# Performance work log

Measured on AMD Instinct MI355X. Metric: run time of the kernel, lower is better.

## Reference

```python
import jax, jax.numpy as jnp
import numpy as np
import math

B, L, D, H, FF = 32, 512, 512, 8, 2048
DH = D // H
EPS = 1e-5

def pe_table(L, D):
    pos = jnp.arange(L, dtype=jnp.float32)[:, None]
    div = jnp.exp(jnp.arange(0, D, 2, dtype=jnp.float32) * (-(math.log(10000.0) / D)))
    pe = jnp.zeros((L, D), dtype=jnp.float32)
    pe = pe.at[:, 0::2].set(jnp.sin(pos * div))
    pe = pe.at[:, 1::2].set(jnp.cos(pos * div))
    return pe

def setup_inputs() -> dict:
    key = jax.random.key(0)
    ks = jax.random.split(key, 16)
    s = 0.02
    inp = {
        "x": jax.random.normal(ks[0], (B, L, D), jnp.float32),
        "mask": jnp.ones((B, L), jnp.int32),
        "speaker_emb": jax.random.normal(ks[1], (B, L, D), jnp.float32),
        "Wg": jax.random.normal(ks[2], (D, D), jnp.float32) * s,
        "Wq": jax.random.normal(ks[3], (D, D), jnp.float32) * s,
        "bq": jnp.zeros((D,), jnp.float32),
        "Wk": jax.random.normal(ks[4], (D, D), jnp.float32) * s,
        "bk": jnp.zeros((D,), jnp.float32),
        "Wv": jax.random.normal(ks[5], (D, D), jnp.float32) * s,
        "bv": jnp.zeros((D,), jnp.float32),
        "Wo": jax.random.normal(ks[6], (D, D), jnp.float32) * s,
        "bo": jnp.zeros((D,), jnp.float32),
        "ln_g": jnp.ones((D,), jnp.float32),
        "ln_b": jnp.zeros((D,), jnp.float32),
        "W1": jax.random.normal(ks[7], (FF, D), jnp.float32) * s,
        "b1": jnp.zeros((FF,), jnp.float32),
        "W2": jax.random.normal(ks[8], (D, FF), jnp.float32) * s,
        "b2": jnp.zeros((D,), jnp.float32),
    }
    return inp

def layer_norm(x, g, b):
    mu = jnp.mean(x, axis=-1, keepdims=True)
    var = jnp.var(x, axis=-1, keepdims=True)
    return (x - mu) * jax.lax.rsqrt(var + EPS) * g + b

def reference(x, mask, speaker_emb, Wg, Wq, bq, Wk, bk, Wv, bv, Wo, bo, ln_g, ln_b, W1, b1, W2, b2):
    # DynamicGating: sigmoid(x W^T) * x
    x = jax.nn.sigmoid(x @ Wg.T) * x
    # speaker embedding + sinusoidal positional encoding (dropout is eval/no-op)
    x = x + speaker_emb + pe_table(L, D)[None, :, :]
    # Multi-head self-attention (eager, full score matrix)
    q = (x @ Wq.T + bq).reshape(B, L, H, DH).transpose(0, 2, 1, 3) / math.sqrt(DH)
    k = (x @ Wk.T + bk).reshape(B, L, H, DH).transpose(0, 2, 1, 3)
    v = (x @ Wv.T + bv).reshape(B, L, H, DH).transpose(0, 2, 1, 3)
    scores = jnp.einsum("bhqd,bhkd->bhqk", q, k)  # (B,H,L,L)
    key_mask = (mask == 0)[:, None, None, :]  # mask keys where mask==0
    scores = jnp.where(key_mask, jnp.float32(-1e10), scores)
    attn = jax.nn.softmax(scores, axis=-1)
    ctx = jnp.einsum("bhqk,bhkd->bhqd", attn, v)
    ctx = ctx.transpose(0, 2, 1, 3).reshape(B, L, D)
    attn_out = ctx @ Wo.T + bo
    h = attn_out + x  # residual (dropout no-op)
    # FeedForwardNet: note GELU applied after BOTH linears (faithful to source)
    mid = jax.nn.gelu(layer_norm(h, ln_g, ln_b) @ W1.T + b1, approximate=True)
    out = jax.nn.gelu(mid @ W2.T + b2, approximate=True)
    return out + h
```

## Files before the change

### kernel.cpp

```cpp
#include <hip/hip_runtime.h>
#include <math.h>

#define Bn 32
#define Ln 512
#define Dn 512
#define Hn 8
#define DHn 64
#define FFn 2048
#define Mn (Bn*Ln)
#define QKVS 1536

typedef __attribute__((ext_vector_type(4))) float f32x4;
typedef __attribute__((ext_vector_type(8))) short short8;

__device__ __forceinline__ float bf2f(ushort u){ return __uint_as_float(((unsigned)u) << 16); }
__device__ __forceinline__ ushort f2bf(float f){
  unsigned u = __float_as_uint(f);
  u += 0x7FFFu + ((u >> 16) & 1u);
  return (ushort)(u >> 16);
}
__device__ __forceinline__ float gelu_fast(float x){
  float y2 = 1.5957691216057308f * (x + 0.044715f*x*x*x);
  return x / (1.0f + __expf(-y2));
}

__device__ __forceinline__ void gload_lds16(const ushort* g, ushort* l){
  __builtin_amdgcn_global_load_lds(
      (__attribute__((address_space(1))) void*)(void*)g,
      (__attribute__((address_space(3))) void*)(void*)l, 16, 0, 0);
}

__device__ __forceinline__ void cvt4(const float* __restrict__ in, ushort* __restrict__ out, int u){
  float4 v = *(const float4*)(in + u*4);
  ushort4 o;
  o.x = f2bf(v.x); o.y = f2bf(v.y); o.z = f2bf(v.z); o.w = f2bf(v.w);
  *(ushort4*)(out + u*4) = o;
}

__global__ __launch_bounds__(256) void prep_kernel(
    const float* __restrict__ Wg, const float* __restrict__ Wq, const float* __restrict__ Wk,
    const float* __restrict__ Wv, const float* __restrict__ Wo, const float* __restrict__ W1,
    const float* __restrict__ W2,
    const float* __restrict__ bq, const float* __restrict__ bk, const float* __restrict__ bv,
    ushort* __restrict__ wgb, ushort* __restrict__ wqkvb, ushort* __restrict__ wob,
    ushort* __restrict__ w1b, ushort* __restrict__ w2b,
    float* __restrict__ pe, float* __restrict__ bqkv)
{
  int u = blockIdx.x*256 + threadIdx.x;
  const int WU = 65536, FU = 262144;
  if (u < WU){ cvt4(Wg, wgb, u); return; }            u -= WU;
  if (u < WU){ cvt4(Wq, wqkvb, u); return; }          u -= WU;
  if (u < WU){ cvt4(Wk, wqkvb + 262144, u); return; } u -= WU;
  if (u < WU){ cvt4(Wv, wqkvb + 524288, u); return; } u -= WU;
  if (u < WU){ cvt4(Wo, wob, u); return; }            u -= WU;
  if (u < FU){ cvt4(W1, w1b, u); return; }            u -= FU;
  if (u < FU){ cvt4(W2, w2b, u); return; }            u -= FU;
  if (u < WU){
    int e = u*4; int l = e >> 9; int d0 = e & 511;
    #pragma unroll
    for (int p=0;p<2;p++){
      int i = (d0 >> 1) + p;
      float dv = expf((float)(2*i) * (-9.210340371976184f/512.0f));
      float ang = (float)l * dv;
      pe[e + 2*p]     = sinf(ang);
      pe[e + 2*p + 1] = cosf(ang);
    }
    return;
  }
  u -= WU;
  if (u < 384){
    int e = u*4;
    #pragma unroll
    for (int j=0;j<4;j++){
      int i = e + j;
      bqkv[i] = (i < 512) ? bq[i] : (i < 1024) ? bk[i-512] : bv[i-1024];
    }
  }
}

__global__ void cvt_kernel(const float* __restrict__ in, ushort* __restrict__ out, int n){
  int i = (blockIdx.x*256 + threadIdx.x)*4;
  if (i >= n) return;
  cvt4(in, out, i >> 2);
}

template<int MODE>
__global__ __launch_bounds__(256) void gemm_kernel(
    const ushort* __restrict__ A, const ushort* __restrict__ W,
    const float* __restrict__ bias,
    const float* __restrict__ res,
    const float* __restrict__ spk, const float* __restrict__ pe,
    float* __restrict__ outf, ushort* __restrict__ outb, ushort* __restrict__ outb2,
    int K, int N, int gx)
{
  __shared__ ushort lA[2][128][64];
  __shared__ ushort lW[2][128][64];
  int t = threadIdx.x;
  int wave = t >> 6, lane = t & 63;
  int wr = wave >> 1, wc = wave & 1;
  int g = lane >> 4, r16 = lane & 15;

  int nwg = gx * (Mn/128);
  int wg = blockIdx.x;
  int tile = (wg & 7)*(nwg >> 3) + (wg >> 3);
  int trow = tile / gx;
  int tcol = tile - trow*gx;
  int rowBase = trow * 128;
  int colBase = tcol * 128;

  int srow8 = lane >> 3;
  int sucol = ((lane & 7) ^ srow8) * 8;
  const ushort* gA = A + (size_t)(rowBase + wave*8 + srow8)*K + sucol;
  const ushort* gW = W + (size_t)(colBase + wave*8 + srow8)*K + sucol;

  f32x4 acc[4][4];
  #pragma unroll
  for (int m=0;m<4;m++)
    #pragma unroll
    for (int n=0;n<4;n++) acc[m][n] = (f32x4)0.0f;

  {
    ushort* la = &lA[0][0][0] + wave*512;
    ushort* lw = &lW[0][0][0] + wave*512;
    #pragma unroll
    for (int c=0;c<4;c++){
      gload_lds16(gA + (size_t)c*32*K, la + c*2048);
      gload_lds16(gW + (size_t)c*32*K, lw + c*2048);
    }
  }

  int cb = 0;
  for (int k0 = 0; k0 < K; k0 += 64){
    if (k0 + 64 < K){
      ushort* la = &lA[cb^1][0][0] + wave*512;
      ushort* lw = &lW[cb^1][0][0] + wave*512;
      #pragma unroll
      for (int c=0;c<4;c++){
        gload_lds16(gA + (size_t)c*32*K + k0 + 64, la + c*2048);
        gload_lds16(gW + (size_t)c*32*K + k0 + 64, lw + c*2048);
      }
      asm volatile("s_waitcnt vmcnt(8)" ::: "memory");
    } else {
      asm volatile("s_waitcnt vmcnt(0)" ::: "memory");
    }
    __builtin_amdgcn_s_barrier();
    #pragma unroll
    for (int ks=0; ks<2; ks++){
      short8 af[4], bfr[4];
      #pragma unroll
      for (int m=0;m<4;m++){
        int row = wr*64 + m*16 + r16;
        af[m] = *(const short8*)&lA[cb][row][(((ks<<2)+g) ^ (r16 & 7))*8];
      }
      #pragma unroll
      for (int n=0;n<4;n++){
        int row = wc*64 + n*16 + r16;
        bfr[n] = *(const short8*)&lW[cb][row][(((ks<<2)+g) ^ (r16 & 7))*8];
      }
      #pragma unroll
      for (int m=0;m<4;m++)
        #pragma unroll
        for (int n=0;n<4;n++)
          acc[m][n] = __builtin_amdgcn_mfma_f32_16x16x32_bf16(af[m], bfr[n], acc[m][n], 0, 0, 0);
    }
    __builtin_amdgcn_s_barrier();
    cb ^= 1;
  }

  if constexpr (MODE == 1 || MODE == 3){
    bool vpart = false;
    if constexpr (MODE == 1) vpart = (colBase >= 1024);
    if (!vpart){
      ushort* ct = &lA[0][0][0];
      #pragma unroll
      for (int m=0;m<4;m++){
        #pragma unroll
        for (int n=0;n<4;n++){
          int col = wc*64 + n*16 + r16;
          int gc = colBase + col;
          float sc = 1.0f;
          if constexpr (MODE == 1) sc = (gc < 512) ? 0.125f : 1.0f;
          #pragma unroll
          for (int j=0;j<4;j++){
            int row = wr*64 + m*16 + g*4 + j;
            float c = acc[m][n][j] + bias[gc];
            ushort val;
            if constexpr (MODE == 3) val = f2bf(gelu_fast(c));
            else                     val = f2bf(c * sc);
            ct[row*128 + (col ^ ((row & 7) << 3))] = val;
          }
        }
      }
      __syncthreads();
      int r = t >> 1, ch = (t & 1)*64;
      ushort* dst = outb + (size_t)(rowBase + r)*N + colBase + ch;
      #pragma unroll
      for (int q=0;q<8;q++){
        int col = (ch + q*8) ^ ((r & 7) << 3);
        *(short8*)(dst + q*8) = *(const short8*)&ct[r*128 + col];
      }
    } else {
      #pragma unroll
      for (int m=0;m<4;m++){
        #pragma unroll
        for (int n=0;n<4;n++){
          int gc = colBase + wc*64 + n*16 + r16;
          int dhg = gc - 1024;
          int gr0 = rowBase + wr*64 + m*16 + g*4;
          int bb = gr0 >> 9, l0 = gr0 & 511;
          ushort4 o4;
          o4.x = f2bf(acc[m][n][0] + bias[gc]);
          o4.y = f2bf(acc[m][n][1] + bias[gc]);
          o4.z = f2bf(acc[m][n][2] + bias[gc]);
          o4.w = f2bf(acc[m][n][3] + bias[gc]);
          *(ushort4*)(outb2 + ((size_t)(bb*Hn + (dhg>>6))*DHn + (dhg & 63))*Ln + l0) = o4;
        }
      }
    }
  } else {
    #pragma unroll
    for (int m=0;m<4;m++){
      #pragma unroll
      for (int n=0;n<4;n++){
        int gc = colBase + wc*64 + n*16 + r16;
        #pragma unroll
        for (int j=0;j<4;j++){
          int gr = rowBase + wr*64 + m*16 + g*4 + j;
          size_t o = (size_t)gr * N + gc;
          float c = acc[m][n][j];
          if constexpr (MODE == 0){
            float s = 1.0f/(1.0f + __expf(-c));
            float rv = s * res[o] + spk[o] + pe[(gr & (Ln-1))*Dn + gc];
            outf[o] = rv; outb[o] = f2bf(rv);
          } else if constexpr (MODE == 2){
            outf[o] = c + bias[gc] + res[o];
          } else {
            outf[o] = gelu_fast(c + bias[gc]) + res[o];
          }
        }
      }
    }
  }
}

__global__ __launch_bounds__(256) void attn_mfma_kernel(
    const ushort* __restrict__ qb, const ushort* __restrict__ kb, const ushort* __restrict__ vtb,
    const int* __restrict__ mask, ushort* __restrict__ ctxb)
{
  __shared__ ushort lK[2][64][72];
  __shared__ ushort lVt[2][64][72];
  __shared__ ushort lP[4][32][72];

  int t = threadIdx.x;
  int w = t >> 6, lane = t & 63;
  int g = lane >> 4, r16 = lane & 15;
  int b = blockIdx.z, h = blockIdx.y;
  int qbase = blockIdx.x*128 + w*32;

  int key0 = t >> 3;
  int c8s = (t & 7) * 8;
  const ushort* kbase = kb + (size_t)(b*Ln)*QKVS + h*DHn + c8s;
  const ushort* vt = vtb + (size_t)((b*Hn + h)*DHn) * Ln;

  short8 af_q[2][2];
  #pragma unroll
  for (int m=0;m<2;m++)
    #pragma unroll
    for (int ks=0;ks<2;ks++)
      af_q[m][ks] = *(const short8*)(qb + (size_t)(b*Ln + qbase + m*16 + r16)*QKVS + h*DHn + ks*32 + g*8);

  f32x4 acc_ctx[2][4];
  #pragma unroll
  for (int m=0;m<2;m++)
    #pragma unroll
    for (int n=0;n<4;n++) acc_ctx[m][n] = (f32x4)0.0f;
  float mrun[2][4], lrun[2][4];
  #pragma unroll
  for (int m=0;m<2;m++)
    #pragma unroll
    for (int j=0;j<4;j++){ mrun[m][j] = -INFINITY; lrun[m][j] = 0.0f; }

  {
    short8 ka = *(const short8*)(kbase + (size_t)key0*QKVS);
    short8 kc = *(const short8*)(kbase + (size_t)(key0+32)*QKVS);
    short8 va = *(const short8*)(vt + (size_t)key0*Ln + c8s);
    short8 vc = *(const short8*)(vt + (size_t)(key0+32)*Ln + c8s);
    *(short8*)&lK[0][key0][c8s] = ka;
    *(short8*)&lK[0][key0+32][c8s] = kc;
    *(short8*)&lVt[0][key0][c8s] = va;
    *(short8*)&lVt[0][key0+32][c8s] = vc;
  }
  __syncthreads();
  int cb = 0;

  for (int kb0 = 0; kb0 < Ln; kb0 += 64){
    short8 kna, knb, vna, vnb;
    bool more = (kb0 + 64 < Ln);
    if (more){
      kna = *(const short8*)(kbase + (size_t)(kb0 + 64 + key0)*QKVS);
      knb = *(const short8*)(kbase + (size_t)(kb0 + 64 + key0 + 32)*QKVS);
      vna = *(const short8*)(vt + (size_t)key0*Ln + kb0 + 64 + c8s);
      vnb = *(const short8*)(vt + (size_t)(key0+32)*Ln + kb0 + 64 + c8s);
    }

    f32x4 acc_s[2][4];
    #pragma unroll
    for (int m=0;m<2;m++)
      #pragma unroll
      for (int n=0;n<4;n++) acc_s[m][n] = (f32x4)0.0f;
    __builtin_amdgcn_s_setprio(1);
    #pragma unroll
    for (int ks=0;ks<2;ks++){
      short8 bf_k[4];
      #pragma unroll
      for (int n=0;n<4;n++)
        bf_k[n] = *(const short8*)&lK[cb][n*16 + r16][ks*32 + g*8];
      #pragma unroll
      for (int m=0;m<2;m++)
        #pragma unroll
        for (int n=0;n<4;n++)
          acc_s[m][n] = __builtin_amdgcn_mfma_f32_16x16x32_bf16(af_q[m][ks], bf_k[n], acc_s[m][n], 0, 0, 0);
    }
    __builtin_amdgcn_s_setprio(0);

    #pragma unroll
    for (int n=0;n<4;n++){
      if (mask[b*Ln + kb0 + n*16 + r16] == 0){
        #pragma unroll
        for (int m=0;m<2;m++)
          #pragma unroll
          for (int j=0;j<4;j++) acc_s[m][n][j] = -1e10f;
      }
    }

    #pragma unroll
    for (int m=0;m<2;m++){
      #pragma unroll
      for (int j=0;j<4;j++){
        float tmax = fmaxf(fmaxf(acc_s[m][0][j], acc_s[m][1][j]),
                           fmaxf(acc_s[m][2][j], acc_s[m][3][j]));
        #pragma unroll
        for (int off=1; off<16; off<<=1) tmax = fmaxf(tmax, __shfl_xor(tmax, off));
        float newm = fmaxf(mrun[m][j], tmax);
        float alpha = __expf(mrun[m][j] - newm);
        float p0 = __expf(acc_s[m][0][j] - newm);
        float p1 = __expf(acc_s[m][1][j] - newm);
        float p2 = __expf(acc_s[m][2][j] - newm);
        float p3 = __expf(acc_s[m][3][j] - newm);
        float tsum = (p0+p1)+(p2+p3);
        #pragma unroll
        for (int off=1; off<16; off<<=1) tsum += __shfl_xor(tsum, off);
        lrun[m][j] = lrun[m][j]*alpha + tsum;
        mrun[m][j] = newm;
        #pragma unroll
        for (int n2=0;n2<4;n2++) acc_ctx[m][n2][j] *= alpha;
        int prow = m*16 + g*4 + j;
        lP[w][prow][0*16 + r16] = f2bf(p0);
        lP[w][prow][1*16 + r16] = f2bf(p1);
        lP[w][prow][2*16 + r16] = f2bf(p2);
        lP[w][prow][3*16 + r16] = f2bf(p3);
      }
    }

    __builtin_amdgcn_s_setprio(1);
    #pragma unroll
    for (int ks2=0;ks2<2;ks2++){
      short8 af_p[2], bf_v[4];
      #pragma unroll
      for (int m=0;m<2;m++)
        af_p[m] = *(const short8*)&lP[w][m*16 + r16][ks2*32 + g*8];
      #pragma unroll
      for (int n=0;n<4;n++)
        bf_v[n] = *(const short8*)&lVt[cb][n*16 + r16][ks2*32 + g*8];
      #pragma unroll
      for (int m=0;m<2;m++)
        #pragma unroll
        for (int n=0;n<4;n++)
          acc_ctx[m][n] = __builtin_amdgcn_mfma_f32_16x16x32_bf16(af_p[m], bf_v[n], acc_ctx[m][n], 0, 0, 0);
    }
    __builtin_amdgcn_s_setprio(0);

    if (more){
      *(short8*)&lK[cb^1][key0][c8s] = kna;
      *(short8*)&lK[cb^1][key0+32][c8s] = knb;
      *(short8*)&lVt[cb^1][key0][c8s] = vna;
      *(short8*)&lVt[cb^1][key0+32][c8s] = vnb;
    }
    __syncthreads();
    cb ^= 1;
  }

  #pragma unroll
  for (int m=0;m<2;m++){
    #pragma unroll
    for (int j=0;j<4;j++){
      float inv = 1.0f / lrun[m][j];
      int gr = qbase + m*16 + g*4 + j;
      #pragma unroll
      for (int n=0;n<4;n++){
        ctxb[(size_t)(b*Ln + gr)*Dn + h*DHn + n*16 + r16] = f2bf(acc_ctx[m][n][j] * inv);
      }
    }
  }
}

__global__ __launch_bounds__(256) void ln_kernel(
    const float* __restrict__ hbuf, const float* __restrict__ gamma, const float* __restrict__ beta,
    ushort* __restrict__ out)
{
  int row = blockIdx.x*4 + (threadIdx.x >> 6);
  int lane = threadIdx.x & 63;
  const float* p = hbuf + (size_t)row*Dn + lane*8;
  float4 a = *(const float4*)p;
  float4 c = *(const float4*)(p + 4);
  float v[8] = {a.x,a.y,a.z,a.w,c.x,c.y,c.z,c.w};
  float s = 0.f, ss = 0.f;
  #pragma unroll
  for (int j=0;j<8;j++){ s += v[j]; ss += v[j]*v[j]; }
  #pragma unroll
  for (int off=32; off>0; off>>=1){ s += __shfl_xor(s, off); ss += __shfl_xor(ss, off); }
  float mu = s * (1.0f/Dn);
  float var = ss * (1.0f/Dn) - mu*mu;
  float rstd = rsqrtf(var + 1e-5f);
  ushort o8[8];
  #pragma unroll
  for (int j=0;j<8;j++) o8[j] = f2bf((v[j]-mu)*rstd*gamma[lane*8+j] + beta[lane*8+j]);
  ushort* op = out + (size_t)row*Dn + lane*8;
  *(ushort4*)op       = make_ushort4(o8[0],o8[1],o8[2],o8[3]);
  *(ushort4*)(op + 4) = make_ushort4(o8[4],o8[5],o8[6],o8[7]);
}

extern "C" void kernel_launch(void* const* d_in, const int* in_sizes, int n_in,
                              void* d_out, int out_size, void* d_ws, size_t ws_size,
                              hipStream_t stream) {
  (void)in_sizes; (void)n_in; (void)out_size; (void)ws_size;
  const float* x    = (const float*)d_in[0];
  const int*   mask = (const int*)d_in[1];
  const float* spk  = (const float*)d_in[2];
  const float* Wg   = (const float*)d_in[3];
  const float* Wq   = (const float*)d_in[4];  const float* bq = (const float*)d_in[5];
  const float* Wk   = (const float*)d_in[6];  const float* bk = (const float*)d_in[7];
  const float* Wv   = (const float*)d_in[8];  const float* bv = (const float*)d_in[9];
  const float* Wo   = (const float*)d_in[10]; const float* bo = (const float*)d_in[11];
  const float* lng  = (const float*)d_in[12]; const float* lnbeta = (const float*)d_in[13];
  const float* W1   = (const float*)d_in[14]; const float* b1 = (const float*)d_in[15];
  const float* W2   = (const float*)d_in[16]; const float* b2 = (const float*)d_in[17];
  float* out = (float*)d_out;

  char* w = (char*)d_ws;
  size_t o = 0;
  ushort* xbf   = (ushort*)(w + o); o += (size_t)Mn*Dn*2;
  ushort* xinb  = (ushort*)(w + o); o += (size_t)Mn*Dn*2;
  ushort* qkvb  = (ushort*)(w + o); o += (size_t)Mn*QKVS*2;
  ushort* vtb   = (ushort*)(w + o); o += (size_t)Mn*Dn*2;
  ushort* ctxb  = (ushort*)(w + o); o += (size_t)Mn*Dn*2;
  float*  xinf  = (float*)(w + o);  o += (size_t)Mn*Dn*4;
  float*  hbuf  = (float*)(w + o);  o += (size_t)Mn*Dn*4;
  ushort* lnbuf = (ushort*)(w + o); o += (size_t)Mn*Dn*2;
  ushort* wgb   = (ushort*)(w + o); o += (size_t)Dn*Dn*2;
  ushort* wqkvb = (ushort*)(w + o); o += (size_t)QKVS*Dn*2;
  ushort* wob   = (ushort*)(w + o); o += (size_t)Dn*Dn*2;
  ushort* w1b   = (ushort*)(w + o); o += (size_t)FFn*Dn*2;
  ushort* w2b   = (ushort*)(w + o); o += (size_t)Dn*FFn*2;
  float*  pebuf = (float*)(w + o);  o += (size_t)Ln*Dn*4;
  float*  bqkv  = (float*)(w + o);  o += (size_t)QKVS*4;
  ushort* midb  = xbf;

  hipLaunchKernelGGL(prep_kernel, dim3(3586), dim3(256), 0, stream,
                     Wg, Wq, Wk, Wv, Wo, W1, W2, bq, bk, bv,
                     wgb, wqkvb, wob, w1b, w2b, pebuf, bqkv);
  hipLaunchKernelGGL(cvt_kernel, dim3((Mn*Dn/4)/256), dim3(256), 0, stream, x, xbf, Mn*Dn);

  hipLaunchKernelGGL((gemm_kernel<0>), dim3((Dn/128)*(Mn/128)), dim3(256), 0, stream,
                     xbf, wgb, (const float*)nullptr, x, spk, pebuf, xinf, xinb, (ushort*)nullptr,
                     Dn, Dn, Dn/128);
  hipLaunchKernelGGL((gemm_kernel<1>), dim3((QKVS/128)*(Mn/128)), dim3(256), 0, stream,
                     xinb, wqkvb, bqkv, (const float*)nullptr, (const float*)nullptr, (const float*)nullptr,
                     (float*)nullptr, qkvb, vtb, Dn, QKVS, QKVS/128);
  hipLaunchKernelGGL(attn_mfma_kernel, dim3(Ln/128, Hn, Bn), dim3(256), 0, stream,
                     qkvb, qkvb + 512, vtb, mask, ctxb);
  hipLaunchKernelGGL((gemm_kernel<2>), dim3((Dn/128)*(Mn/128)), dim3(256), 0, stream,
                     ctxb, wob, bo, xinf, (const float*)nullptr, (const float*)nullptr,
                     hbuf, (ushort*)nullptr, (ushort*)nullptr, Dn, Dn, Dn/128);
  hipLaunchKernelGGL(ln_kernel, dim3(Mn/4), dim3(256), 0, stream, hbuf, lng, lnbeta, lnbuf);
  hipLaunchKernelGGL((gemm_kernel<3>), dim3((FFn/128)*(Mn/128)), dim3(256), 0, stream,
                     lnbuf, w1b, b1, (const float*)nullptr, (const float*)nullptr, (const float*)nullptr,
                     (float*)nullptr, midb, (ushort*)nullptr, Dn, FFn, FFn/128);
  hipLaunchKernelGGL((gemm_kernel<4>), dim3((Dn/128)*(Mn/128)), dim3(256), 0, stream,
                     midb, w2b, b2, hbuf, (const float*)nullptr, (const float*)nullptr,
                     out, (ushort*)nullptr, (ushort*)nullptr, FFn, Dn, Dn/128);
}
```

Before: 324.5 us.

## Enlarge GEMM tiles to 256x256 with 8 waves and drop fp32 residual copy

The GEMM kernel moves from 128x128 tiles with 4 waves to 256x256 tiles with 8 waves, each wave computing a 128x64 sub-tile. This raises arithmetic intensity and cuts global reloads of A and W. The gating GEMM now writes only a bf16 result through the LDS-staged epilogue. The Wo GEMM reads that bf16 copy as its residual, removing a full fp32 write and read of the activation. In exchange the grid has fewer workgroups, which may hurt occupancy on small GEMMs, registers rise, and the residual loses precision by going through bf16.

```diff
diff --git a/kernel.cpp b/kernel.cpp
--- a/kernel.cpp
+++ b/kernel.cpp
@@ -85,59 +85,53 @@
 }
 
 template<int MODE>
-__global__ __launch_bounds__(256) void gemm_kernel(
+__global__ __launch_bounds__(512) void gemm_kernel(
     const ushort* __restrict__ A, const ushort* __restrict__ W,
     const float* __restrict__ bias,
     const float* __restrict__ res,
+    const ushort* __restrict__ rbf,
     const float* __restrict__ spk, const float* __restrict__ pe,
     float* __restrict__ outf, ushort* __restrict__ outb, ushort* __restrict__ outb2,
     int K, int N, int gx)
 {
-  __shared__ ushort lA[2][128][64];
-  __shared__ ushort lW[2][128][64];
+  __shared__ ushort lbuf[2][2][16384];
   int t = threadIdx.x;
   int wave = t >> 6, lane = t & 63;
-  int wr = wave >> 1, wc = wave & 1;
+  int wrow = wave >> 2, wcol = wave & 3;
   int g = lane >> 4, r16 = lane & 15;
 
-  int nwg = gx * (Mn/128);
+  int nwg = gx * (Mn/256);
   int wg = blockIdx.x;
   int tile = (wg & 7)*(nwg >> 3) + (wg >> 3);
   int trow = tile / gx;
   int tcol = tile - trow*gx;
-  int rowBase = trow * 128;
-  int colBase = tcol * 128;
+  int rowBase = trow * 256;
+  int colBase = tcol * 256;
 
   int srow8 = lane >> 3;
   int sucol = ((lane & 7) ^ srow8) * 8;
   const ushort* gA = A + (size_t)(rowBase + wave*8 + srow8)*K + sucol;
   const ushort* gW = W + (size_t)(colBase + wave*8 + srow8)*K + sucol;
 
-  f32x4 acc[4][4];
-  #pragma unroll
-  for (int m=0;m<4;m++)
+  f32x4 acc[8][4];
+  #pragma unroll
+  for (int m=0;m<8;m++)
     #pragma unroll
     for (int n=0;n<4;n++) acc[m][n] = (f32x4)0.0f;
 
-  {
-    ushort* la = &lA[0][0][0] + wave*512;
-    ushort* lw = &lW[0][0][0] + wave*512;
-    #pragma unroll
-    for (int c=0;c<4;c++){
-      gload_lds16(gA + (size_t)c*32*K, la + c*2048);
-      gload_lds16(gW + (size_t)c*32*K, lw + c*2048);
-    }
+  #pragma unroll
+  for (int c=0;c<4;c++){
+    gload_lds16(gA + (size_t)c*64*K, &lbuf[0][0][c*4096 + wave*512]);
+    gload_lds16(gW + (size_t)c*64*K, &lbuf[0][1][c*4096 + wave*512]);
   }
 
   int cb = 0;
   for (int k0 = 0; k0 < K; k0 += 64){
     if (k0 + 64 < K){
-      ushort* la = &lA[cb^1][0][0] + wave*512;
-      ushort* lw = &lW[cb^1][0][0] + wave*512;
       #pragma unroll
       for (int c=0;c<4;c++){
-        gload_lds16(gA + (size_t)c*32*K + k0 + 64, la + c*2048);
-        gload_lds16(gW + (size_t)c*32*K + k0 + 64, lw + c*2048);
+        gload_lds16(gA + (size_t)c*64*K + k0 + 64, &lbuf[cb^1][0][c*4096 + wave*512]);
+        gload_lds16(gW + (size_t)c*64*K + k0 + 64, &lbuf[cb^1][1][c*4096 + wave*512]);
       }
       asm volatile("s_waitcnt vmcnt(8)" ::: "memory");
     } else {
@@ -146,19 +140,19 @@
     __builtin_amdgcn_s_barrier();
     #pragma unroll
     for (int ks=0; ks<2; ks++){
-      short8 af[4], bfr[4];
-      #pragma unroll
-      for (int m=0;m<4;m++){
-        int row = wr*64 + m*16 + r16;
-        af[m] = *(const short8*)&lA[cb][row][(((ks<<2)+g) ^ (r16 & 7))*8];
+      short8 af[8], bfr[4];
+      #pragma unroll
+      for (int m=0;m<8;m++){
+        int row = wrow*128 + m*16 + r16;
+        af[m] = *(const short8*)&lbuf[cb][0][row*64 + (((ks<<2)+g) ^ (r16 & 7))*8];
       }
       #pragma unroll
       for (int n=0;n<4;n++){
-        int row = wc*64 + n*16 + r16;
-        bfr[n] = *(const short8*)&lW[cb][row][(((ks<<2)+g) ^ (r16 & 7))*8];
-      }
-      #pragma unroll
-      for (int m=0;m<4;m++)
+        int row = wcol*64 + n*16 + r16;
+        bfr[n] = *(const short8*)&lbuf[cb][1][row*64 + (((ks<<2)+g) ^ (r16 & 7))*8];
+      }
+      #pragma unroll
+      for (int m=0;m<8;m++)
         #pragma unroll
         for (int n=0;n<4;n++)
           acc[m][n] = __builtin_amdgcn_mfma_f32_16x16x32_bf16(af[m], bfr[n], acc[m][n], 0, 0, 0);
@@ -167,46 +161,54 @@
     cb ^= 1;
   }
 
-  if constexpr (MODE == 1 || MODE == 3){
+  if constexpr (MODE == 0 || MODE == 1 || MODE == 3){
     bool vpart = false;
     if constexpr (MODE == 1) vpart = (colBase >= 1024);
     if (!vpart){
-      ushort* ct = &lA[0][0][0];
-      #pragma unroll
-      for (int m=0;m<4;m++){
+      ushort* ct = &lbuf[0][0][0];
+      #pragma unroll
+      for (int m=0;m<8;m++){
         #pragma unroll
         for (int n=0;n<4;n++){
-          int col = wc*64 + n*16 + r16;
+          int col = wcol*64 + n*16 + r16;
           int gc = colBase + col;
           float sc = 1.0f;
           if constexpr (MODE == 1) sc = (gc < 512) ? 0.125f : 1.0f;
           #pragma unroll
           for (int j=0;j<4;j++){
-            int row = wr*64 + m*16 + g*4 + j;
-            float c = acc[m][n][j] + bias[gc];
+            int row = wrow*128 + m*16 + g*4 + j;
+            float c = acc[m][n][j];
             ushort val;
-            if constexpr (MODE == 3) val = f2bf(gelu_fast(c));
-            else                     val = f2bf(c * sc);
-            ct[row*128 + (col ^ ((row & 7) << 3))] = val;
+            if constexpr (MODE == 0){
+              int gr = rowBase + row;
+              size_t o = (size_t)gr * N + gc;
+              float s = 1.0f/(1.0f + __expf(-c));
+              val = f2bf(s * res[o] + spk[o] + pe[(gr & (Ln-1))*Dn + gc]);
+            } else if constexpr (MODE == 3){
+              val = f2bf(gelu_fast(c + bias[gc]));
+            } else {
+              val = f2bf((c + bias[gc]) * sc);
+            }
+            ct[row*256 + (col ^ ((row & 7) << 3))] = val;
           }
         }
       }
       __syncthreads();
-      int r = t >> 1, ch = (t & 1)*64;
+      int r = t >> 1, ch = (t & 1)*128;
       ushort* dst = outb + (size_t)(rowBase + r)*N + colBase + ch;
       #pragma unroll
-      for (int q=0;q<8;q++){
+      for (int q=0;q<16;q++){
         int col = (ch + q*8) ^ ((r & 7) << 3);
-        *(short8*)(dst + q*8) = *(const short8*)&ct[r*128 + col];
+        *(short8*)(dst + q*8) = *(const short8*)&ct[r*256 + col];
       }
     } else {
       #pragma unroll
-      for (int m=0;m<4;m++){
+      for (int m=0;m<8;m++){
         #pragma unroll
         for (int n=0;n<4;n++){
-          int gc = colBase + wc*64 + n*16 + r16;
+          int gc = colBase + wcol*64 + n*16 + r16;
           int dhg = gc - 1024;
-          int gr0 = rowBase + wr*64 + m*16 + g*4;
+          int gr0 = rowBase + wrow*128 + m*16 + g*4;
           int bb = gr0 >> 9, l0 = gr0 & 511;
           ushort4 o4;
           o4.x = f2bf(acc[m][n][0] + bias[gc]);
@@ -219,21 +221,17 @@
     }
   } else {
     #pragma unroll
-    for (int m=0;m<4;m++){
+    for (int m=0;m<8;m++){
       #pragma unroll
       for (int n=0;n<4;n++){
-        int gc = colBase + wc*64 + n*16 + r16;
+        int gc = colBase + wcol*64 + n*16 + r16;
         #pragma unroll
         for (int j=0;j<4;j++){
-          int gr = rowBase + wr*64 + m*16 + g*4 + j;
+          int gr = rowBase + wrow*128 + m*16 + g*4 + j;
           size_t o = (size_t)gr * N + gc;
           float c = acc[m][n][j];
-          if constexpr (MODE == 0){
-            float s = 1.0f/(1.0f + __expf(-c));
-            float rv = s * res[o] + spk[o] + pe[(gr & (Ln-1))*Dn + gc];
-            outf[o] = rv; outb[o] = f2bf(rv);
-          } else if constexpr (MODE == 2){
-            outf[o] = c + bias[gc] + res[o];
+          if constexpr (MODE == 2){
+            outf[o] = c + bias[gc] + bf2f(rbf[o]);
           } else {
             outf[o] = gelu_fast(c + bias[gc]) + res[o];
           }
@@ -454,7 +452,6 @@
   ushort* qkvb  = (ushort*)(w + o); o += (size_t)Mn*QKVS*2;
   ushort* vtb   = (ushort*)(w + o); o += (size_t)Mn*Dn*2;
   ushort* ctxb  = (ushort*)(w + o); o += (size_t)Mn*Dn*2;
-  float*  xinf  = (float*)(w + o);  o += (size_t)Mn*Dn*4;
   float*  hbuf  = (float*)(w + o);  o += (size_t)Mn*Dn*4;
   ushort* lnbuf = (ushort*)(w + o); o += (size_t)Mn*Dn*2;
   ushort* wgb   = (ushort*)(w + o); o += (size_t)Dn*Dn*2;
@@ -471,22 +468,25 @@
                      wgb, wqkvb, wob, w1b, w2b, pebuf, bqkv);
   hipLaunchKernelGGL(cvt_kernel, dim3((Mn*Dn/4)/256), dim3(256), 0, stream, x, xbf, Mn*Dn);
 
-  hipLaunchKernelGGL((gemm_kernel<0>), dim3((Dn/128)*(Mn/128)), dim3(256), 0, stream,
-                     xbf, wgb, (const float*)nullptr, x, spk, pebuf, xinf, xinb, (ushort*)nullptr,
-                     Dn, Dn, Dn/128);
-  hipLaunchKernelGGL((gemm_kernel<1>), dim3((QKVS/128)*(Mn/128)), dim3(256), 0, stream,
-                     xinb, wqkvb, bqkv, (const float*)nullptr, (const float*)nullptr, (const float*)nullptr,
-                     (float*)nullptr, qkvb, vtb, Dn, QKVS, QKVS/128);
+  hipLaunchKernelGGL((gemm_kernel<0>), dim3((Dn/256)*(Mn/256)), dim3(512), 0, stream,
+                     xbf, wgb, (const float*)nullptr, x, (const ushort*)nullptr, spk, pebuf,
+                     (float*)nullptr, xinb, (ushort*)nullptr, Dn, Dn, Dn/256);
+  hipLaunchKernelGGL((gemm_kernel<1>), dim3((QKVS/256)*(Mn/256)), dim3(512), 0, stream,
+                     xinb, wqkvb, bqkv, (const float*)nullptr, (const ushort*)nullptr,
+                     (const float*)nullptr, (const float*)nullptr,
+                     (float*)nullptr, qkvb, vtb, Dn, QKVS, QKVS/256);
   hipLaunchKernelGGL(attn_mfma_kernel, dim3(Ln/128, Hn, Bn), dim3(256), 0, stream,
                      qkvb, qkvb + 512, vtb, mask, ctxb);
-  hipLaunchKernelGGL((gemm_kernel<2>), dim3((Dn/128)*(Mn/128)), dim3(256), 0, stream,
-                     ctxb, wob, bo, xinf, (const float*)nullptr, (const float*)nullptr,
-                     hbuf, (ushort*)nullptr, (ushort*)nullptr, Dn, Dn, Dn/128);
+  hipLaunchKernelGGL((gemm_kernel<2>), dim3((Dn/256)*(Mn/256)), dim3(512), 0, stream,
+                     ctxb, wob, bo, (const float*)nullptr, xinb, (const float*)nullptr,
+                     (const float*)nullptr, hbuf, (ushort*)nullptr, (ushort*)nullptr, Dn, Dn, Dn/256);
   hipLaunchKernelGGL(ln_kernel, dim3(Mn/4), dim3(256), 0, stream, hbuf, lng, lnbeta, lnbuf);
-  hipLaunchKernelGGL((gemm_kernel<3>), dim3((FFn/128)*(Mn/128)), dim3(256), 0, stream,
-                     lnbuf, w1b, b1, (const float*)nullptr, (const float*)nullptr, (const float*)nullptr,
-                     (float*)nullptr, midb, (ushort*)nullptr, Dn, FFn, FFn/128);
-  hipLaunchKernelGGL((gemm_kernel<4>), dim3((Dn/128)*(Mn/128)), dim3(256), 0, stream,
-                     midb, w2b, b2, hbuf, (const float*)nullptr, (const float*)nullptr,
-                     out, (ushort*)nullptr, (ushort*)nullptr, FFn, Dn, Dn/128);
-}
+  hipLaunchKernelGGL((gemm_kernel<3>), dim3((FFn/256)*(Mn/256)), dim3(512), 0, stream,
+                     lnbuf, w1b, b1, (const float*)nullptr, (const ushort*)nullptr,
+                     (const float*)nullptr, (const float*)nullptr,
+                     (float*)nullptr, midb, (ushort*)nullptr, Dn, FFn, FFn/256);
+  hipLaunchKernelGGL((gemm_kernel<4>), dim3((Dn/256)*(Mn/256)), dim3(512), 0, stream,
+                     midb, w2b, b2, hbuf, (const ushort*)nullptr,
+                     (const float*)nullptr, (const float*)nullptr,
+                     out, (ushort*)nullptr, (ushort*)nullptr, FFn, Dn, Dn/256);
+}
```

Result: slower. 347.3 us (+7.0%).
